# Kernel tuning notes

Hardware: AMD Instinct MI355X
Metric: run time of the kernel (lower is better)

Reference implementation:

```python
import jax, jax.numpy as jnp
import numpy as np

NQ = 10          # qubits
NT = 32          # tokens (LCU terms)
DM = 512         # d_model
DEG = 2          # qsvt degree
B = 128          # batch
NPQC = 4 * NQ    # params per PQC application
DIM = 2 ** NQ    # statevector dimension


def ansatz14_spec(q, layers=1):
    spec = []
    for _ in range(layers):
        spec += [('ry', (i,)) for i in range(q)]
        spec += [('crx', (i, (i + 1) % q)) for i in range(q - 1, -1, -1)]
        spec += [('ry', (i,)) for i in range(q)]
        spec += [('crx', (i, (i - 1) % q)) for i in [q - 1] + list(range(q - 1))]
    return spec

SPEC = ansatz14_spec(NQ, 1)


def _gate_ry(theta):
    h = theta * 0.5
    c = jnp.cos(h)
    s = jnp.sin(h)
    m = jnp.stack([jnp.stack([c, -s], -1), jnp.stack([s, c], -1)], -2)
    return m.astype(jnp.complex64)  # (N,2,2)


def _gate_rx(theta):
    h = theta * 0.5
    c = jnp.cos(h).astype(jnp.complex64)
    s = (-1j) * jnp.sin(h).astype(jnp.complex64)
    return jnp.stack([jnp.stack([c, s], -1), jnp.stack([s, c], -1)], -2)


def _apply_1q(state, mats, wire, q):
    # state: (N, 2^q) complex; mats: (N,2,2); wire 0 is most significant bit
    N = state.shape[0]
    a = 2 ** wire
    bdim = 2 ** (q - wire - 1)
    s = state.reshape(N, a, 2, bdim)
    return jnp.einsum('nij,najb->naib', mats, s).reshape(N, 2 ** q)


def _apply_crx(state, theta, c, t, q):
    # controlled-RX: control wire c, target wire t
    N = state.shape[0]
    st = state.reshape((N,) + (2,) * q)
    ax = 1 + c
    s0 = jnp.take(st, 0, axis=ax)   # control = 0 branch: untouched
    s1 = jnp.take(st, 1, axis=ax)   # control = 1 branch: apply RX on target
    tp = t if t < c else t - 1      # target wire position after removing control axis
    s1n = _apply_1q(s1.reshape(N, -1), _gate_rx(theta), tp, q - 1).reshape(s1.shape)
    return jnp.stack([s0, s1n], axis=ax).reshape(N, 2 ** q)


def _apply_pqc(state, params, q):
    # params: (N, NPQC); fixed small gate list -> Python loop is fine
    for k, (fn, w) in enumerate(SPEC):
        th = params[:, k]
        if fn == 'ry':
            state = _apply_1q(state, _gate_ry(th), w[0], q)
        else:
            state = _apply_crx(state, th, w[0], w[1], q)
    return state


def _apply_lcu(states, params, lcu):
    # states: (B, DIM) complex; params: (B, L, NPQC); lcu: (B, L) complex
    Bn, L = lcu.shape
    rep = jnp.repeat(states, L, axis=0)                    # (B*L, DIM)
    st = _apply_pqc(rep, params.reshape(Bn * L, NPQC), NQ)
    return jnp.einsum('bld,bl->bd', st.reshape(Bn, L, DIM), lcu)


def _measure_xyz(state, q):
    # Pauli expectations per wire: order [X_0..X_{q-1}, Y_0.., Z_0..]
    N = state.shape[0]
    xs, ys, zs = [], [], []
    for w in range(q):
        s = state.reshape(N, 2 ** w, 2, -1)
        a0, a1 = s[:, :, 0, :], s[:, :, 1, :]
        cross = jnp.sum(jnp.conj(a0) * a1, axis=(1, 2))
        xs.append(2.0 * jnp.real(cross))
        ys.append(2.0 * jnp.imag(cross))
        zs.append(jnp.sum(jnp.abs(a0) ** 2 - jnp.abs(a1) ** 2, axis=(1, 2)))
    return jnp.stack(xs + ys + zs, axis=1).astype(jnp.float32)  # (B, 3q)


def reference(tokens_emb, W, b, lcu_re, lcu_im, qsvt_coeffs, ff_params):
    Bn, L, D = tokens_emb.shape
    L = min(L, NT)
    pqc_params = tokens_emb[:, :L] @ W.T + b               # (B, L, NPQC)
    lcu = (lcu_re + 1j * lcu_im).astype(jnp.complex64)[:L]
    lcu = lcu / jnp.sum(jnp.abs(lcu))
    lcu_b = jnp.broadcast_to(lcu[None], (Bn, L))
    init = jnp.zeros((Bn, DIM), jnp.complex64).at[:, 0].set(1.0)
    acc = qsvt_coeffs[0].astype(jnp.complex64) * init
    mono = init
    for k in range(1, DEG + 1):
        mono = _apply_lcu(mono, pqc_params, lcu_b)
        acc = acc + qsvt_coeffs[k].astype(jnp.complex64) * mono
    state = acc / jnp.sum(jnp.abs(qsvt_coeffs))
    state = state / jnp.linalg.norm(state, axis=-1, keepdims=True)
    ffp = jnp.broadcast_to(ff_params[None], (Bn, NPQC))
    state = _apply_pqc(state, ffp, NQ)
    return _measure_xyz(state, NQ)


def setup_inputs():
    key = jax.random.key(0)
    ks = jax.random.split(key, 7)
    return {
        'tokens_emb': jax.random.normal(ks[0], (B, NT, DM), jnp.float32),
        'W': jax.random.normal(ks[1], (NPQC, DM), jnp.float32) * 0.05,
        'b': jax.random.normal(ks[2], (NPQC,), jnp.float32),
        'lcu_re': jax.random.normal(ks[3], (NT,), jnp.float32),
        'lcu_im': jax.random.normal(ks[4], (NT,), jnp.float32),
        'qsvt_coeffs': jax.random.normal(ks[5], (DEG + 1,), jnp.float32),
        'ff_params': jax.random.normal(ks[6], (NPQC,), jnp.float32),
    }
```

## Files before the change

kernel.cpp:

```cpp
#include <hip/hip_runtime.h>
#include <hip/hip_bf16.h>


#define NQ   10
#define NT   32
#define DM   512
#define BATCH 128
#define NPQC 40
#define DIM  1024
#define SLICE_V2F (BATCH * DIM)

typedef float v2f __attribute__((ext_vector_type(2)));

#define WAITLDS asm volatile("s_waitcnt lgkmcnt(0)" ::: "memory")

__device__ __forceinline__ v2f Jrot(v2f v) {
  return __builtin_shufflevector(v, -v, 1, 2);
}
__device__ __forceinline__ v2f Jc(v2f v) {
  return __builtin_shufflevector(-v, v, 1, 2);
}


template<int B>
__device__ __forceinline__ void g_ry(v2f (&a)[16], float c, float s) {
  static_assert(B >= 6, "RY targets must be register bits");
  constexpr int m = 1 << (B - 6);
#pragma unroll
  for (int r = 0; r < 16; ++r) {
    if (!(r & m)) {
      int r1 = r | m;
      v2f a0 = a[r], a1 = a[r1];
      a[r]  = c * a0 - s * a1;
      a[r1] = s * a0 + c * a1;
    }
  }
}

template<int BC, int BT>
__device__ __forceinline__ void g_crx(v2f (&a)[16], int lane, float c, float s) {
  static_assert(BT >= 6, "CRX targets must be register bits");
  constexpr int m = 1 << (BT - 6);
  bool lane_ok = (BC >= 6) || ((lane >> BC) & 1);
  float ce = lane_ok ? c : 1.f;
  float se = lane_ok ? s : 0.f;
#pragma unroll
  for (int r = 0; r < 16; ++r) {
    if (!(r & m)) {
      if constexpr (BC >= 6) { if (!((r >> (BC - 6)) & 1)) continue; }
      int r1 = r | m;
      v2f a0 = a[r], a1 = a[r1];
      a[r]  = ce * a0 + se * Jrot(a1);
      a[r1] = ce * a1 + se * Jrot(a0);
    }
  }
}

template<int L0, int L1, int L2, int L3>
__device__ __forceinline__ void remap(v2f (&a)[16], v2f* __restrict__ slab,
                                      int lane) {
  constexpr int LM = (1 << L0) | (1 << L1) | (1 << L2) | (1 << L3);
#pragma unroll
  for (int r = 0; r < 16; ++r) {
    int f = 0;
    if (L0 < 4 && (r & 1)) f |= 1 << L0;
    if (L1 < 4 && (r & 2)) f |= 1 << L1;
    if (L2 < 4 && (r & 4)) f |= 1 << L2;
    if (L3 < 4 && (r & 8)) f |= 1 << L3;
    slab[r * 64 + (lane ^ f)] = a[r];
  }
  WAITLDS;
  int la = lane & ~LM & 63;
  la |= ((lane >> L0) & 1) << 6;
  la |= ((lane >> L1) & 1) << 7;
  la |= ((lane >> L2) & 1) << 8;
  la |= ((lane >> L3) & 1) << 9;
  if (L0 < 4) la |= ((lane >> L0) & 1) << L0;
  if (L1 < 4) la |= ((lane >> L1) & 1) << L1;
  if (L2 < 4) la |= ((lane >> L2) & 1) << L2;
  if (L3 < 4) la |= ((lane >> L3) & 1) << L3;
#pragma unroll
  for (int r = 0; r < 16; ++r) {
    int rc = ((r & 1) ? (1 << L0) : 0) | ((r & 2) ? (1 << L1) : 0)
           | ((r & 4) ? (1 << L2) : 0) | ((r & 8) ? (1 << L3) : 0);
    a[r] = slab[la ^ rc];
  }
}

template<bool SKIP_HEAD>
__device__ __forceinline__ void apply_pqc_phased(v2f (&a)[16],
    const float2* __restrict__ cs, v2f* __restrict__ slab, int lane) {
#define RYt(B, t)      g_ry<B>(a, t.x, t.y);
#define CXt(BC, BT, t) g_crx<BC, BT>(a, lane, t.x, t.y);
  float2 t10 = cs[10], t11 = cs[11], t12 = cs[12];
  if constexpr (!SKIP_HEAD) {
    float2 t0 = cs[0], t1 = cs[1], t2 = cs[2], t3 = cs[3];
    float2 t4 = cs[4], t5 = cs[5], t6 = cs[6], t7 = cs[7];
    float2 t8 = cs[8], t9 = cs[9];
    RYt(9,t0) RYt(8,t1) RYt(7,t2) RYt(6,t3)
    remap<5,4,3,2>(a, slab, lane);
    RYt(6,t4) RYt(7,t5) RYt(8,t6) RYt(9,t7)
    remap<1,0,2,3>(a, slab, lane);
    RYt(6,t8) RYt(7,t9)
  }
  CXt(7,8,t10) CXt(6,7,t11) CXt(3,6,t12)
  float2 t13 = cs[13], t14 = cs[14], t15 = cs[15], t16 = cs[16];
  remap<1,0,2,3>(a, slab, lane);
  CXt(8,9,t13) CXt(7,8,t14) CXt(6,7,t15) CXt(5,6,t16)
  float2 t17 = cs[17], t18 = cs[18], t19 = cs[19];
  float2 t20 = cs[20], t21 = cs[21], t22 = cs[22], t23 = cs[23];
  remap<2,3,4,5>(a, slab, lane);
  CXt(8,9,t17) CXt(7,8,t18) CXt(6,7,t19)
  RYt(6,t20) RYt(7,t21) RYt(8,t22) RYt(9,t23)
  float2 t24 = cs[24], t25 = cs[25], t26 = cs[26], t27 = cs[27];
  remap<2,3,4,5>(a, slab, lane);
  RYt(6,t24) RYt(7,t25) RYt(8,t26) RYt(9,t27)
  float2 t28 = cs[28], t29 = cs[29];
  float2 t30 = cs[30], t31 = cs[31], t32 = cs[32], t33 = cs[33];
  remap<1,0,2,3>(a, slab, lane);
  RYt(6,t28) RYt(7,t29)
  CXt(7,6,t30) CXt(8,7,t31) CXt(9,8,t32) CXt(4,9,t33)
  float2 t34 = cs[34], t35 = cs[35], t36 = cs[36], t37 = cs[37];
  remap<4,5,1,0>(a, slab, lane);
  CXt(7,6,t34) CXt(8,7,t35) CXt(9,8,t36) CXt(2,9,t37)
  float2 t38 = cs[38], t39 = cs[39];
  remap<2,3,4,5>(a, slab, lane);
  CXt(7,6,t38) CXt(8,7,t39)
#undef RYt
#undef CXt
}

__device__ __forceinline__ int p8_lane_canon(int lane) {
  return (((lane >> 1) & 1) << 9) | ((lane & 1) << 8) | (((lane >> 2) & 1) << 7)
       | (((lane >> 3) & 1) << 6) | (((lane >> 4) & 1) << 5) | (((lane >> 5) & 1) << 4);
}

__device__ __forceinline__ void stagger(int key) {
  int s = key & 3;
  if (s & 1) __builtin_amdgcn_s_sleep(1);
  if (s & 2) __builtin_amdgcn_s_sleep(2);
}

__global__ __launch_bounds__(256) void params_kernel(
    const float* __restrict__ emb, const float* __restrict__ W,
    const float* __restrict__ bias,
    const float* __restrict__ lcu_re, const float* __restrict__ lcu_im,
    const float* __restrict__ ffp,
    float2* __restrict__ cs, float2* __restrict__ ffcs, float2* __restrict__ lcu,
    v2f* __restrict__ part1, v2f* __restrict__ part2) {
  int blk = blockIdx.x;
  int tid = threadIdx.x;
  if (blk >= 257) {
    int idx = (blk - 257) * 256 + tid;
    v2f z = (v2f)(0.f);
    if (idx < SLICE_V2F) part1[idx] = z;
    else                 part2[idx - SLICE_V2F] = z;
    return;
  }
  if (blk == 256) {
    if (tid < NPQC) {
      float h = 0.5f * ffp[tid];
      ffcs[tid] = make_float2(cosf(h), sinf(h));
    }
    if (tid == 64) {
      float ssum = 0.f;
      for (int i = 0; i < NT; ++i) {
        float re = lcu_re[i], im = lcu_im[i];
        ssum += sqrtf(re * re + im * im);
      }
      float inv = 1.f / ssum;
      for (int i = 0; i < NT; ++i)
        lcu[i] = make_float2(lcu_re[i] * inv, lcu_im[i] * inv);
    }
    return;
  }

  __shared__ float Asl[16 * 516];
  int row0 = blk * 16;

  const float4* eg = (const float4*)(emb + (size_t)row0 * DM);
#pragma unroll
  for (int i = 0; i < 8; ++i) {
    int e = tid + i * 256;
    int r = e >> 7, k4 = e & 127;
    float4 v = eg[e];
    *(float4*)&Asl[r * 516 + k4 * 4] = v;
  }
  __syncthreads();

  int kq = tid >> 6;
  int lane = tid & 63;
  int rg = lane >> 3;
  int cg = lane & 7;

  const float* Ar0 = &Asl[(2 * rg) * 516 + kq * 128];
  const float* Ar1 = Ar0 + 516;
  const float* Bg  = W + (size_t)(5 * cg) * DM + kq * 128;

  float acc[2][5] = {};
#pragma unroll 4
  for (int k = 0; k < 128; k += 4) {
    float4 a0 = *(const float4*)(Ar0 + k);
    float4 a1 = *(const float4*)(Ar1 + k);
#pragma unroll
    for (int j = 0; j < 5; ++j) {
      float4 b = *(const float4*)(Bg + j * DM + k);
      acc[0][j] += a0.x * b.x + a0.y * b.y + a0.z * b.z + a0.w * b.w;
      acc[1][j] += a1.x * b.x + a1.y * b.y + a1.z * b.z + a1.w * b.w;
    }
  }

  __syncthreads();
  float* red = Asl;
#pragma unroll
  for (int i = 0; i < 2; ++i)
#pragma unroll
    for (int j = 0; j < 5; ++j)
      red[kq * 644 + (2 * rg + i) * 40 + 5 * cg + j] = acc[i][j];
  __syncthreads();

  for (int o = tid; o < 640; o += 256) {
    float v = bias[o % 40] + red[o] + red[644 + o] + red[1288 + o] + red[1932 + o];
    float h = 0.5f * v;
    cs[(size_t)blk * 640 + o] = make_float2(cosf(h), sinf(h));
  }
}

template<bool FIRST>
__global__ __launch_bounds__(256) void pqc_step(
    const float2* __restrict__ cs, const float2* __restrict__ lcu,
    const v2f* __restrict__ src, v2f* __restrict__ dst) {
  __shared__ v2f slabs[4][1024];
  int tid = threadIdx.x;
  int lane = tid & 63;
  int wvu = __builtin_amdgcn_readfirstlane(tid >> 6);
  int blk = blockIdx.x;
  stagger(blk + wvu);
  int b = blk >> 3, qq = blk & 7;
  int l = qq * 4 + wvu;
  const float2* csrow = cs + (size_t)(b * NT + l) * NPQC;
  v2f* slab = slabs[wvu];

  v2f a[16];
  if constexpr (FIRST) {
    float2 f5 = csrow[5], f4 = csrow[4], f6 = csrow[6], f7 = csrow[7];
    float2 f2 = csrow[2], f3 = csrow[3];
    float2 f8 = csrow[8], f9 = csrow[9], f0 = csrow[0], f1 = csrow[1];
    float lp = ((lane & 1) ? f5.y : f5.x);
    lp *= ((lane & 2) ? f4.y : f4.x);
    lp *= ((lane & 4) ? f6.y : f6.x);
    lp *= ((lane & 8) ? f7.y : f7.x);
    lp *= ((lane & 16) ? f2.y : f2.x);
    lp *= ((lane & 32) ? f3.y : f3.x);
#pragma unroll
    for (int r = 0; r < 16; ++r) {
      float rp = ((r & 1) ? f8.y : f8.x) * ((r & 2) ? f9.y : f9.x)
               * ((r & 4) ? f0.y : f0.x) * ((r & 8) ? f1.y : f1.x);
      a[r].x = lp * rp;
      a[r].y = 0.f;
    }
  } else {
    const v2f* s = src + (size_t)b * DIM;
#pragma unroll
    for (int r = 0; r < 16; ++r) a[r] = s[r * 64 + lane];
  }

  apply_pqc_phased<FIRST>(a, csrow, slab, lane);

  float2 w = lcu[l];
  int pl = p8_lane_canon(lane);
  pl ^= (pl >> 5);
#pragma unroll
  for (int r = 0; r < 16; ++r) {
    int rc = ((r & 1) << 3) | ((r & 2) << 1) | ((r & 4) >> 1) | ((r & 8) >> 3);
    slab[pl ^ rc] = w.x * a[r] + w.y * Jc(a[r]);
  }
  __syncthreads();

  float* df = (float*)(dst + (size_t)b * DIM);
#pragma unroll
  for (int i = 0; i < 4; ++i) {
    int n = tid + i * 256;
    int ph = n ^ (n >> 5);
    v2f sum = slabs[0][ph] + slabs[1][ph] + slabs[2][ph] + slabs[3][ph];
    atomicAdd(df + 2 * n,     sum.x);
    atomicAdd(df + 2 * n + 1, sum.y);
  }
}

__global__ __launch_bounds__(256) void final_fused(
    const v2f* __restrict__ red1, const v2f* __restrict__ red2b,
    const float* __restrict__ qsvt, const float2* __restrict__ ffcs,
    float* __restrict__ out) {
  __shared__ v2f st[1024];
  __shared__ float2 ang[40];
  __shared__ float rbuf[4];
  __shared__ float red2[120];
  int b = blockIdx.x, tid = threadIdx.x;
  int lane = tid & 63, wvu = tid >> 6;
  float q0 = qsvt[0], q1 = qsvt[1], q2 = qsvt[2];
  const v2f* r1 = red1 + (size_t)b * DIM;
  const v2f* p2 = red2b + (size_t)b * DIM;

  if (tid < NPQC) ang[tid] = ffcs[tid];

  v2f vals[4];
  float nn = 0.f;
#pragma unroll
  for (int i = 0; i < 4; ++i) {
    int n = tid + i * 256;
    v2f v = q1 * r1[n] + q2 * p2[n];
    if (n == 0) v.x += q0;
    vals[i] = v;
    nn += v.x * v.x + v.y * v.y;
  }
#pragma unroll
  for (int o = 1; o < 64; o <<= 1) nn += __shfl_xor(nn, o);
  if (lane == 0) rbuf[wvu] = nn;
  __syncthreads();
  float inv = 1.f / sqrtf(rbuf[0] + rbuf[1] + rbuf[2] + rbuf[3]);
#pragma unroll
  for (int i = 0; i < 4; ++i) {
    int n = tid + i * 256;
    st[n ^ (n >> 5)] = vals[i] * inv;
  }
  __syncthreads();

#pragma unroll 1
  for (int k = 0; k < NPQC; ++k) {
    int isCrx, c, t;
    if (k < 10)      { isCrx = 0; t = k;      c = 0; }
    else if (k < 20) { int i = 19 - k; isCrx = 1; c = i; t = (i == 9) ? 0 : i + 1; }
    else if (k < 30) { isCrx = 0; t = k - 20; c = 0; }
    else             { int i = (k == 30) ? 9 : k - 31; isCrx = 1; c = i; t = (i == 0) ? 9 : i - 1; }
    int m  = 1 << (9 - t);
    int cb = 9 - c;
    float2 th = ang[k];
    float cg = th.x, sg = th.y;

    v2f a0[2], a1[2];
    int j0[2], j1[2], en[2];
#pragma unroll
    for (int p = 0; p < 2; ++p) {
      int qp = p * 256 + tid;
      int i0 = ((qp & ~(m - 1)) << 1) | (qp & (m - 1));
      int i1 = i0 | m;
      j0[p] = i0 ^ (i0 >> 5);
      j1[p] = i1 ^ (i1 >> 5);
      en[p] = (i0 >> cb) & 1;
      a0[p] = st[j0[p]];
      a1[p] = st[j1[p]];
    }
#pragma unroll
    for (int p = 0; p < 2; ++p) {
      v2f n0, n1;
      if (!isCrx) {
        n0 = cg * a0[p] - sg * a1[p];
        n1 = sg * a0[p] + cg * a1[p];
      } else {
        float ce = en[p] ? cg : 1.f;
        float se = en[p] ? sg : 0.f;
        n0 = ce * a0[p] + se * Jrot(a1[p]);
        n1 = ce * a1[p] + se * Jrot(a0[p]);
      }
      st[j0[p]] = n0;
      st[j1[p]] = n1;
    }
    __syncthreads();
  }

  float prt[30];
#pragma unroll
  for (int w = 0; w < NQ; ++w) {
    int m = 1 << (9 - w);
    float xr = 0.f, xi = 0.f, zz = 0.f;
#pragma unroll
    for (int p = 0; p < 2; ++p) {
      int qp = p * 256 + tid;
      int i0 = ((qp & ~(m - 1)) << 1) | (qp & (m - 1));
      int i1 = i0 | m;
      v2f a0 = st[i0 ^ (i0 >> 5)];
      v2f a1 = st[i1 ^ (i1 >> 5)];
      xr += a0.x * a1.x + a0.y * a1.y;
      xi += a0.x * a1.y - a0.y * a1.x;
      zz += a0.x * a0.x + a0.y * a0.y - a1.x * a1.x - a1.y * a1.y;
    }
    prt[w]      = xr;
    prt[10 + w] = xi;
    prt[20 + w] = zz;
  }
#pragma unroll
  for (int v = 0; v < 30; ++v) {
#pragma unroll
    for (int o = 1; o < 64; o <<= 1) prt[v] += __shfl_xor(prt[v], o);
  }
  if (lane == 0) {
#pragma unroll
    for (int v = 0; v < 30; ++v) red2[wvu * 30 + v] = prt[v];
  }
  __syncthreads();
  if (tid < 30) {
    float s2 = red2[tid] + red2[30 + tid] + red2[60 + tid] + red2[90 + tid];
    float sc = (tid < 20) ? 2.f : 1.f;
    out[b * 30 + tid] = sc * s2;
  }
}


extern "C" void kernel_launch(void* const* d_in, const int* in_sizes, int n_in,
                              void* d_out, int out_size, void* d_ws, size_t ws_size,
                              hipStream_t stream) {
  const float* emb    = (const float*)d_in[0];
  const float* W      = (const float*)d_in[1];
  const float* bias   = (const float*)d_in[2];
  const float* lcu_re = (const float*)d_in[3];
  const float* lcu_im = (const float*)d_in[4];
  const float* qsvt   = (const float*)d_in[5];
  const float* ffp    = (const float*)d_in[6];
  float* out = (float*)d_out;

  char* ws = (char*)d_ws;
  float2* cs    = (float2*)ws;
  float2* ffcs  = (float2*)(ws + 1310720);
  float2* lcu   = (float2*)(ws + 1311040);
  v2f*    part1 = (v2f*)(ws + 1311744);
  v2f*    part2 = (v2f*)(ws + 1311744 + 1048576);

  params_kernel<<<1281, 256, 0, stream>>>(emb, W, bias, lcu_re, lcu_im, ffp,
                                          cs, ffcs, lcu, part1, part2);
  pqc_step<true><<<1024, 256, 0, stream>>>(cs, lcu, nullptr, part1);
  pqc_step<false><<<1024, 256, 0, stream>>>(cs, lcu, part1, part2);
  final_fused<<<BATCH, 256, 0, stream>>>(part1, part2, qsvt, ffcs, out);
}
```

Before: 148.3 us.

## Replace LDS remap-phased circuit with runtime gate loop using cross-lane shuffles

Replaces the statically scheduled PQC application, which periodically remapped qubit bits between lanes and registers through LDS, with a non-unrolled runtime loop over the 40 gates. Gates on register bits use templated register kernels chosen by switch, and gates on lane bits use __shfl_xor exchanges. This removes the LDS remap traffic and the stagger sleeps, but adds a runtime gate-decode loop with branches, and many shuffles (16 registers × 2 floats per lane-bit gate) that may cost more than the removed remaps. The canonical layout is now fixed, so the initial product state and the final LDS store order are adjusted to match.

```diff
diff --git a/kernel.cpp b/kernel.cpp
--- a/kernel.cpp
+++ b/kernel.cpp
@@ -12,8 +12,6 @@
 
 typedef float v2f __attribute__((ext_vector_type(2)));
 
-#define WAITLDS asm volatile("s_waitcnt lgkmcnt(0)" ::: "memory")
-
 __device__ __forceinline__ v2f Jrot(v2f v) {
   return __builtin_shufflevector(v, -v, 1, 2);
 }
@@ -22,14 +20,12 @@
 }
 
 
-template<int B>
-__device__ __forceinline__ void g_ry(v2f (&a)[16], float c, float s) {
-  static_assert(B >= 6, "RY targets must be register bits");
-  constexpr int m = 1 << (B - 6);
+template<int M>
+__device__ __forceinline__ void ry_reg(v2f (&a)[16], float c, float s) {
 #pragma unroll
   for (int r = 0; r < 16; ++r) {
-    if (!(r & m)) {
-      int r1 = r | m;
+    if (!(r & M)) {
+      int r1 = r | M;
       v2f a0 = a[r], a1 = a[r1];
       a[r]  = c * a0 - s * a1;
       a[r1] = s * a0 + c * a1;
@@ -37,18 +33,16 @@
   }
 }
 
-template<int BC, int BT>
-__device__ __forceinline__ void g_crx(v2f (&a)[16], int lane, float c, float s) {
-  static_assert(BT >= 6, "CRX targets must be register bits");
-  constexpr int m = 1 << (BT - 6);
-  bool lane_ok = (BC >= 6) || ((lane >> BC) & 1);
-  float ce = lane_ok ? c : 1.f;
-  float se = lane_ok ? s : 0.f;
+template<int M>
+__device__ __forceinline__ void crx_reg(v2f (&a)[16], int lane, int cb,
+                                        float c, float s) {
 #pragma unroll
   for (int r = 0; r < 16; ++r) {
-    if (!(r & m)) {
-      if constexpr (BC >= 6) { if (!((r >> (BC - 6)) & 1)) continue; }
-      int r1 = r | m;
+    if (!(r & M)) {
+      int r1 = r | M;
+      int en = (cb >= 6) ? ((r >> (cb - 6)) & 1) : ((lane >> cb) & 1);
+      float ce = en ? c : 1.f;
+      float se = en ? s : 0.f;
       v2f a0 = a[r], a1 = a[r1];
       a[r]  = ce * a0 + se * Jrot(a1);
       a[r1] = ce * a1 + se * Jrot(a0);
@@ -56,89 +50,80 @@
   }
 }
 
-template<int L0, int L1, int L2, int L3>
-__device__ __forceinline__ void remap(v2f (&a)[16], v2f* __restrict__ slab,
-                                      int lane) {
-  constexpr int LM = (1 << L0) | (1 << L1) | (1 << L2) | (1 << L3);
-#pragma unroll
-  for (int r = 0; r < 16; ++r) {
-    int f = 0;
-    if (L0 < 4 && (r & 1)) f |= 1 << L0;
-    if (L1 < 4 && (r & 2)) f |= 1 << L1;
-    if (L2 < 4 && (r & 4)) f |= 1 << L2;
-    if (L3 < 4 && (r & 8)) f |= 1 << L3;
-    slab[r * 64 + (lane ^ f)] = a[r];
-  }
-  WAITLDS;
-  int la = lane & ~LM & 63;
-  la |= ((lane >> L0) & 1) << 6;
-  la |= ((lane >> L1) & 1) << 7;
-  la |= ((lane >> L2) & 1) << 8;
-  la |= ((lane >> L3) & 1) << 9;
-  if (L0 < 4) la |= ((lane >> L0) & 1) << L0;
-  if (L1 < 4) la |= ((lane >> L1) & 1) << L1;
-  if (L2 < 4) la |= ((lane >> L2) & 1) << L2;
-  if (L3 < 4) la |= ((lane >> L3) & 1) << L3;
-#pragma unroll
-  for (int r = 0; r < 16; ++r) {
-    int rc = ((r & 1) ? (1 << L0) : 0) | ((r & 2) ? (1 << L1) : 0)
-           | ((r & 4) ? (1 << L2) : 0) | ((r & 8) ? (1 << L3) : 0);
-    a[r] = slab[la ^ rc];
-  }
-}
-
-template<bool SKIP_HEAD>
-__device__ __forceinline__ void apply_pqc_phased(v2f (&a)[16],
-    const float2* __restrict__ cs, v2f* __restrict__ slab, int lane) {
-#define RYt(B, t)      g_ry<B>(a, t.x, t.y);
-#define CXt(BC, BT, t) g_crx<BC, BT>(a, lane, t.x, t.y);
-  float2 t10 = cs[10], t11 = cs[11], t12 = cs[12];
-  if constexpr (!SKIP_HEAD) {
-    float2 t0 = cs[0], t1 = cs[1], t2 = cs[2], t3 = cs[3];
-    float2 t4 = cs[4], t5 = cs[5], t6 = cs[6], t7 = cs[7];
-    float2 t8 = cs[8], t9 = cs[9];
-    RYt(9,t0) RYt(8,t1) RYt(7,t2) RYt(6,t3)
-    remap<5,4,3,2>(a, slab, lane);
-    RYt(6,t4) RYt(7,t5) RYt(8,t6) RYt(9,t7)
-    remap<1,0,2,3>(a, slab, lane);
-    RYt(6,t8) RYt(7,t9)
-  }
-  CXt(7,8,t10) CXt(6,7,t11) CXt(3,6,t12)
-  float2 t13 = cs[13], t14 = cs[14], t15 = cs[15], t16 = cs[16];
-  remap<1,0,2,3>(a, slab, lane);
-  CXt(8,9,t13) CXt(7,8,t14) CXt(6,7,t15) CXt(5,6,t16)
-  float2 t17 = cs[17], t18 = cs[18], t19 = cs[19];
-  float2 t20 = cs[20], t21 = cs[21], t22 = cs[22], t23 = cs[23];
-  remap<2,3,4,5>(a, slab, lane);
-  CXt(8,9,t17) CXt(7,8,t18) CXt(6,7,t19)
-  RYt(6,t20) RYt(7,t21) RYt(8,t22) RYt(9,t23)
-  float2 t24 = cs[24], t25 = cs[25], t26 = cs[26], t27 = cs[27];
-  remap<2,3,4,5>(a, slab, lane);
-  RYt(6,t24) RYt(7,t25) RYt(8,t26) RYt(9,t27)
-  float2 t28 = cs[28], t29 = cs[29];
-  float2 t30 = cs[30], t31 = cs[31], t32 = cs[32], t33 = cs[33];
-  remap<1,0,2,3>(a, slab, lane);
-  RYt(6,t28) RYt(7,t29)
-  CXt(7,6,t30) CXt(8,7,t31) CXt(9,8,t32) CXt(4,9,t33)
-  float2 t34 = cs[34], t35 = cs[35], t36 = cs[36], t37 = cs[37];
-  remap<4,5,1,0>(a, slab, lane);
-  CXt(7,6,t34) CXt(8,7,t35) CXt(9,8,t36) CXt(2,9,t37)
-  float2 t38 = cs[38], t39 = cs[39];
-  remap<2,3,4,5>(a, slab, lane);
-  CXt(7,6,t38) CXt(8,7,t39)
-#undef RYt
-#undef CXt
-}
-
-__device__ __forceinline__ int p8_lane_canon(int lane) {
-  return (((lane >> 1) & 1) << 9) | ((lane & 1) << 8) | (((lane >> 2) & 1) << 7)
-       | (((lane >> 3) & 1) << 6) | (((lane >> 4) & 1) << 5) | (((lane >> 5) & 1) << 4);
-}
-
-__device__ __forceinline__ void stagger(int key) {
-  int s = key & 3;
-  if (s & 1) __builtin_amdgcn_s_sleep(1);
-  if (s & 2) __builtin_amdgcn_s_sleep(2);
+template<int K0>
+__device__ __forceinline__ void run_circuit(v2f (&a)[16],
+    const float2* __restrict__ angs, int lane) {
+  float2 th = angs[K0];
+#pragma unroll 1
+  for (int k = K0; k < NPQC; ++k) {
+    float2 thn = angs[(k + 1 < NPQC) ? k + 1 : k];
+    int isCrx, tb, cb;
+    {
+      int c, t;
+      if (k < 10)      { isCrx = 0; t = k;      c = 0; }
+      else if (k < 20) { int i = 19 - k; isCrx = 1; c = i; t = (i == 9) ? 0 : i + 1; }
+      else if (k < 30) { isCrx = 0; t = k - 20; c = 0; }
+      else             { int i = (k == 30) ? 9 : k - 31; isCrx = 1; c = i; t = (i == 0) ? 9 : i - 1; }
+      tb = 9 - t;
+      cb = 9 - c;
+    }
+    float cg = th.x, sg = th.y;
+
+    if (tb >= 6) {
+      if (!isCrx) {
+        switch (tb) {
+          case 6:  ry_reg<1>(a, cg, sg); break;
+          case 7:  ry_reg<2>(a, cg, sg); break;
+          case 8:  ry_reg<4>(a, cg, sg); break;
+          default: ry_reg<8>(a, cg, sg); break;
+        }
+      } else {
+        switch (tb) {
+          case 6:  crx_reg<1>(a, lane, cb, cg, sg); break;
+          case 7:  crx_reg<2>(a, lane, cb, cg, sg); break;
+          case 8:  crx_reg<4>(a, lane, cb, cg, sg); break;
+          default: crx_reg<8>(a, lane, cb, cg, sg); break;
+        }
+      }
+    } else {
+      int lm = 1 << tb;
+      if (!isCrx) {
+        int bit = (lane >> tb) & 1;
+        float ss = bit ? sg : -sg;
+#pragma unroll
+        for (int r = 0; r < 16; ++r) {
+          float px = __shfl_xor(a[r].x, lm);
+          float py = __shfl_xor(a[r].y, lm);
+          a[r].x = cg * a[r].x + ss * px;
+          a[r].y = cg * a[r].y + ss * py;
+        }
+      } else if (cb < 6) {
+        int en = (lane >> cb) & 1;
+        float ce = en ? cg : 1.f;
+        float se = en ? sg : 0.f;
+#pragma unroll
+        for (int r = 0; r < 16; ++r) {
+          float px = __shfl_xor(a[r].x, lm);
+          float py = __shfl_xor(a[r].y, lm);
+          a[r].x = ce * a[r].x + se * py;
+          a[r].y = ce * a[r].y - se * px;
+        }
+      } else {
+        int csh = cb - 6;
+#pragma unroll
+        for (int r = 0; r < 16; ++r) {
+          float px = __shfl_xor(a[r].x, lm);
+          float py = __shfl_xor(a[r].y, lm);
+          int en = (r >> csh) & 1;
+          float ce = en ? cg : 1.f;
+          float se = en ? sg : 0.f;
+          a[r].x = ce * a[r].x + se * py;
+          a[r].y = ce * a[r].y - se * px;
+        }
+      }
+    }
+    th = thn;
+  }
 }
 
 __global__ __launch_bounds__(256) void params_kernel(
@@ -235,7 +220,6 @@
   int lane = tid & 63;
   int wvu = __builtin_amdgcn_readfirstlane(tid >> 6);
   int blk = blockIdx.x;
-  stagger(blk + wvu);
   int b = blk >> 3, qq = blk & 7;
   int l = qq * 4 + wvu;
   const float2* csrow = cs + (size_t)(b * NT + l) * NPQC;
@@ -243,19 +227,19 @@
 
   v2f a[16];
   if constexpr (FIRST) {
-    float2 f5 = csrow[5], f4 = csrow[4], f6 = csrow[6], f7 = csrow[7];
-    float2 f2 = csrow[2], f3 = csrow[3];
-    float2 f8 = csrow[8], f9 = csrow[9], f0 = csrow[0], f1 = csrow[1];
-    float lp = ((lane & 1) ? f5.y : f5.x);
-    lp *= ((lane & 2) ? f4.y : f4.x);
-    lp *= ((lane & 4) ? f6.y : f6.x);
-    lp *= ((lane & 8) ? f7.y : f7.x);
-    lp *= ((lane & 16) ? f2.y : f2.x);
-    lp *= ((lane & 32) ? f3.y : f3.x);
+    float2 f9 = csrow[9], f8 = csrow[8], f7 = csrow[7], f6 = csrow[6];
+    float2 f5 = csrow[5], f4 = csrow[4], f3 = csrow[3], f2 = csrow[2];
+    float2 f1 = csrow[1], f0 = csrow[0];
+    float lp = ((lane & 1) ? f9.y : f9.x);
+    lp *= ((lane & 2)  ? f8.y : f8.x);
+    lp *= ((lane & 4)  ? f7.y : f7.x);
+    lp *= ((lane & 8)  ? f6.y : f6.x);
+    lp *= ((lane & 16) ? f5.y : f5.x);
+    lp *= ((lane & 32) ? f4.y : f4.x);
 #pragma unroll
     for (int r = 0; r < 16; ++r) {
-      float rp = ((r & 1) ? f8.y : f8.x) * ((r & 2) ? f9.y : f9.x)
-               * ((r & 4) ? f0.y : f0.x) * ((r & 8) ? f1.y : f1.x);
+      float rp = ((r & 1) ? f3.y : f3.x) * ((r & 2) ? f2.y : f2.x)
+               * ((r & 4) ? f1.y : f1.x) * ((r & 8) ? f0.y : f0.x);
       a[r].x = lp * rp;
       a[r].y = 0.f;
     }
@@ -265,15 +249,13 @@
     for (int r = 0; r < 16; ++r) a[r] = s[r * 64 + lane];
   }
 
-  apply_pqc_phased<FIRST>(a, csrow, slab, lane);
+  run_circuit<FIRST ? 10 : 0>(a, csrow, lane);
 
   float2 w = lcu[l];
-  int pl = p8_lane_canon(lane);
-  pl ^= (pl >> 5);
 #pragma unroll
   for (int r = 0; r < 16; ++r) {
-    int rc = ((r & 1) << 3) | ((r & 2) << 1) | ((r & 4) >> 1) | ((r & 8) >> 3);
-    slab[pl ^ rc] = w.x * a[r] + w.y * Jc(a[r]);
+    int n = r * 64 + lane;
+    slab[n ^ (n >> 5)] = w.x * a[r] + w.y * Jc(a[r]);
   }
   __syncthreads();
 
```

After: 193.0 us. 1.3x slower.

## Fuse final PQC and measurement into second pqc_step via last-block counter

Applied to the files above, without the earlier changes.

Removes the separate final kernel by having the last of the eight blocks per batch row, detected with an atomic counter, run the normalization, feed-forward PQC and measurement inside the second pqc_step. The counters are zeroed in params_kernel. This saves a kernel launch and the gap between kernels, and lets the tail work for one batch row overlap with other rows still accumulating. In exchange it adds a threadfence, atomic reads of the accumulated buffer, and a serialized tail inside the last block of each row.

```diff
diff --git a/kernel.cpp b/kernel.cpp
--- a/kernel.cpp
+++ b/kernel.cpp
@@ -147,7 +147,7 @@
     const float* __restrict__ lcu_re, const float* __restrict__ lcu_im,
     const float* __restrict__ ffp,
     float2* __restrict__ cs, float2* __restrict__ ffcs, float2* __restrict__ lcu,
-    v2f* __restrict__ part1, v2f* __restrict__ part2) {
+    v2f* __restrict__ part1, v2f* __restrict__ part2, int* __restrict__ cnt) {
   int blk = blockIdx.x;
   int tid = threadIdx.x;
   if (blk >= 257) {
@@ -162,6 +162,7 @@
       float h = 0.5f * ffp[tid];
       ffcs[tid] = make_float2(cosf(h), sinf(h));
     }
+    if (tid >= 128) cnt[tid - 128] = 0;
     if (tid == 64) {
       float ssum = 0.f;
       for (int i = 0; i < NT; ++i) {
@@ -229,8 +230,11 @@
 template<bool FIRST>
 __global__ __launch_bounds__(256) void pqc_step(
     const float2* __restrict__ cs, const float2* __restrict__ lcu,
-    const v2f* __restrict__ src, v2f* __restrict__ dst) {
+    const v2f* __restrict__ src, v2f* __restrict__ dst,
+    const float* __restrict__ qsvt, const float2* __restrict__ ffcs,
+    float* __restrict__ out, int* __restrict__ cnt) {
   __shared__ v2f slabs[4][1024];
+  __shared__ int lastFlag;
   int tid = threadIdx.x;
   int lane = tid & 63;
   int wvu = __builtin_amdgcn_readfirstlane(tid >> 6);
@@ -286,123 +290,131 @@
     atomicAdd(df + 2 * n,     sum.x);
     atomicAdd(df + 2 * n + 1, sum.y);
   }
-}
-
-__global__ __launch_bounds__(256) void final_fused(
-    const v2f* __restrict__ red1, const v2f* __restrict__ red2b,
-    const float* __restrict__ qsvt, const float2* __restrict__ ffcs,
-    float* __restrict__ out) {
-  __shared__ v2f st[1024];
-  __shared__ float2 ang[40];
-  __shared__ float rbuf[4];
-  __shared__ float red2[120];
-  int b = blockIdx.x, tid = threadIdx.x;
-  int lane = tid & 63, wvu = tid >> 6;
-  float q0 = qsvt[0], q1 = qsvt[1], q2 = qsvt[2];
-  const v2f* r1 = red1 + (size_t)b * DIM;
-  const v2f* p2 = red2b + (size_t)b * DIM;
-
-  if (tid < NPQC) ang[tid] = ffcs[tid];
-
-  v2f vals[4];
-  float nn = 0.f;
-#pragma unroll
-  for (int i = 0; i < 4; ++i) {
-    int n = tid + i * 256;
-    v2f v = q1 * r1[n] + q2 * p2[n];
-    if (n == 0) v.x += q0;
-    vals[i] = v;
-    nn += v.x * v.x + v.y * v.y;
-  }
-#pragma unroll
-  for (int o = 1; o < 64; o <<= 1) nn += __shfl_xor(nn, o);
-  if (lane == 0) rbuf[wvu] = nn;
-  __syncthreads();
-  float inv = 1.f / sqrtf(rbuf[0] + rbuf[1] + rbuf[2] + rbuf[3]);
-#pragma unroll
-  for (int i = 0; i < 4; ++i) {
-    int n = tid + i * 256;
-    st[n ^ (n >> 5)] = vals[i] * inv;
-  }
-  __syncthreads();
+
+  if constexpr (!FIRST) {
+    __threadfence();
+    if (tid == 0) {
+      int old = atomicAdd(&cnt[b], 1);
+      lastFlag = (old == 7);
+    }
+    __syncthreads();
+    if (!lastFlag) return;
+
+    v2f* st = slabs[0];
+    float* aux = (float*)slabs[1];
+    float2* ang = (float2*)aux;
+    float* rbuf = aux + 80;
+    float* red2 = aux + 96;
+
+    if (tid < NPQC) ang[tid] = ffcs[tid];
+    float q0 = qsvt[0], q1 = qsvt[1], q2 = qsvt[2];
+    const v2f* r1 = src + (size_t)b * DIM;
+
+    v2f vals[4];
+    float nn = 0.f;
+#pragma unroll
+    for (int i = 0; i < 4; ++i) {
+      int n = tid + i * 256;
+      float mx = atomicAdd(df + 2 * n,     0.f);
+      float my = atomicAdd(df + 2 * n + 1, 0.f);
+      v2f r = r1[n];
+      v2f v;
+      v.x = q1 * r.x + q2 * mx;
+      v.y = q1 * r.y + q2 * my;
+      if (n == 0) v.x += q0;
+      vals[i] = v;
+      nn += v.x * v.x + v.y * v.y;
+    }
+#pragma unroll
+    for (int o = 1; o < 64; o <<= 1) nn += __shfl_xor(nn, o);
+    if (lane == 0) rbuf[wvu] = nn;
+    __syncthreads();
+    float inv = 1.f / sqrtf(rbuf[0] + rbuf[1] + rbuf[2] + rbuf[3]);
+#pragma unroll
+    for (int i = 0; i < 4; ++i) {
+      int n = tid + i * 256;
+      st[n ^ (n >> 5)] = vals[i] * inv;
+    }
+    __syncthreads();
 
 #pragma unroll 1
-  for (int k = 0; k < NPQC; ++k) {
-    int isCrx, c, t;
-    if (k < 10)      { isCrx = 0; t = k;      c = 0; }
-    else if (k < 20) { int i = 19 - k; isCrx = 1; c = i; t = (i == 9) ? 0 : i + 1; }
-    else if (k < 30) { isCrx = 0; t = k - 20; c = 0; }
-    else             { int i = (k == 30) ? 9 : k - 31; isCrx = 1; c = i; t = (i == 0) ? 9 : i - 1; }
-    int m  = 1 << (9 - t);
-    int cb = 9 - c;
-    float2 th = ang[k];
-    float cg = th.x, sg = th.y;
-
-    v2f a0[2], a1[2];
-    int j0[2], j1[2], en[2];
-#pragma unroll
-    for (int p = 0; p < 2; ++p) {
-      int qp = p * 256 + tid;
-      int i0 = ((qp & ~(m - 1)) << 1) | (qp & (m - 1));
-      int i1 = i0 | m;
-      j0[p] = i0 ^ (i0 >> 5);
-      j1[p] = i1 ^ (i1 >> 5);
-      en[p] = (i0 >> cb) & 1;
-      a0[p] = st[j0[p]];
-      a1[p] = st[j1[p]];
-    }
-#pragma unroll
-    for (int p = 0; p < 2; ++p) {
-      v2f n0, n1;
-      if (!isCrx) {
-        n0 = cg * a0[p] - sg * a1[p];
-        n1 = sg * a0[p] + cg * a1[p];
-      } else {
-        float ce = en[p] ? cg : 1.f;
-        float se = en[p] ? sg : 0.f;
-        n0 = ce * a0[p] + se * Jrot(a1[p]);
-        n1 = ce * a1[p] + se * Jrot(a0[p]);
+    for (int k = 0; k < NPQC; ++k) {
+      int isCrx, c, t;
+      if (k < 10)      { isCrx = 0; t = k;      c = 0; }
+      else if (k < 20) { int i = 19 - k; isCrx = 1; c = i; t = (i == 9) ? 0 : i + 1; }
+      else if (k < 30) { isCrx = 0; t = k - 20; c = 0; }
+      else             { int i = (k == 30) ? 9 : k - 31; isCrx = 1; c = i; t = (i == 0) ? 9 : i - 1; }
+      int m  = 1 << (9 - t);
+      int cb = 9 - c;
+      float2 th = ang[k];
+      float cg = th.x, sg = th.y;
+
+      v2f a0[2], a1[2];
+      int j0[2], j1[2], en[2];
+#pragma unroll
+      for (int p = 0; p < 2; ++p) {
+        int qp = p * 256 + tid;
+        int i0 = ((qp & ~(m - 1)) << 1) | (qp & (m - 1));
+        int i1 = i0 | m;
+        j0[p] = i0 ^ (i0 >> 5);
+        j1[p] = i1 ^ (i1 >> 5);
+        en[p] = (i0 >> cb) & 1;
+        a0[p] = st[j0[p]];
+        a1[p] = st[j1[p]];
       }
-      st[j0[p]] = n0;
-      st[j1[p]] = n1;
+#pragma unroll
+      for (int p = 0; p < 2; ++p) {
+        v2f n0, n1;
+        if (!isCrx) {
+          n0 = cg * a0[p] - sg * a1[p];
+          n1 = sg * a0[p] + cg * a1[p];
+        } else {
+          float ce = en[p] ? cg : 1.f;
+          float se = en[p] ? sg : 0.f;
+          n0 = ce * a0[p] + se * Jrot(a1[p]);
+          n1 = ce * a1[p] + se * Jrot(a0[p]);
+        }
+        st[j0[p]] = n0;
+        st[j1[p]] = n1;
+      }
+      __syncthreads();
+    }
+
+    float prt[30];
+#pragma unroll
+    for (int w2 = 0; w2 < NQ; ++w2) {
+      int m = 1 << (9 - w2);
+      float xr = 0.f, xi = 0.f, zz = 0.f;
+#pragma unroll
+      for (int p = 0; p < 2; ++p) {
+        int qp = p * 256 + tid;
+        int i0 = ((qp & ~(m - 1)) << 1) | (qp & (m - 1));
+        int i1 = i0 | m;
+        v2f a0 = st[i0 ^ (i0 >> 5)];
+        v2f a1 = st[i1 ^ (i1 >> 5)];
+        xr += a0.x * a1.x + a0.y * a1.y;
+        xi += a0.x * a1.y - a0.y * a1.x;
+        zz += a0.x * a0.x + a0.y * a0.y - a1.x * a1.x - a1.y * a1.y;
+      }
+      prt[w2]      = xr;
+      prt[10 + w2] = xi;
+      prt[20 + w2] = zz;
+    }
+#pragma unroll
+    for (int v = 0; v < 30; ++v) {
+#pragma unroll
+      for (int o = 1; o < 64; o <<= 1) prt[v] += __shfl_xor(prt[v], o);
+    }
+    if (lane == 0) {
+#pragma unroll
+      for (int v = 0; v < 30; ++v) red2[wvu * 30 + v] = prt[v];
     }
     __syncthreads();
-  }
-
-  float prt[30];
-#pragma unroll
-  for (int w = 0; w < NQ; ++w) {
-    int m = 1 << (9 - w);
-    float xr = 0.f, xi = 0.f, zz = 0.f;
-#pragma unroll
-    for (int p = 0; p < 2; ++p) {
-      int qp = p * 256 + tid;
-      int i0 = ((qp & ~(m - 1)) << 1) | (qp & (m - 1));
-      int i1 = i0 | m;
-      v2f a0 = st[i0 ^ (i0 >> 5)];
-      v2f a1 = st[i1 ^ (i1 >> 5)];
-      xr += a0.x * a1.x + a0.y * a1.y;
-      xi += a0.x * a1.y - a0.y * a1.x;
-      zz += a0.x * a0.x + a0.y * a0.y - a1.x * a1.x - a1.y * a1.y;
-    }
-    prt[w]      = xr;
-    prt[10 + w] = xi;
-    prt[20 + w] = zz;
-  }
-#pragma unroll
-  for (int v = 0; v < 30; ++v) {
-#pragma unroll
-    for (int o = 1; o < 64; o <<= 1) prt[v] += __shfl_xor(prt[v], o);
-  }
-  if (lane == 0) {
-#pragma unroll
-    for (int v = 0; v < 30; ++v) red2[wvu * 30 + v] = prt[v];
-  }
-  __syncthreads();
-  if (tid < 30) {
-    float s2 = red2[tid] + red2[30 + tid] + red2[60 + tid] + red2[90 + tid];
-    float sc = (tid < 20) ? 2.f : 1.f;
-    out[b * 30 + tid] = sc * s2;
+    if (tid < 30) {
+      float s2 = red2[tid] + red2[30 + tid] + red2[60 + tid] + red2[90 + tid];
+      float sc = (tid < 20) ? 2.f : 1.f;
+      out[b * 30 + tid] = sc * s2;
+    }
   }
 }
 
@@ -425,10 +437,12 @@
   float2* lcu   = (float2*)(ws + 1311040);
   v2f*    part1 = (v2f*)(ws + 1311744);
   v2f*    part2 = (v2f*)(ws + 1311744 + 1048576);
+  int*    cnt   = (int*)(ws + 1311744 + 2 * 1048576);
 
   params_kernel<<<1281, 256, 0, stream>>>(emb, W, bias, lcu_re, lcu_im, ffp,
-                                          cs, ffcs, lcu, part1, part2);
-  pqc_step<true><<<1024, 256, 0, stream>>>(cs, lcu, nullptr, part1);
-  pqc_step<false><<<1024, 256, 0, stream>>>(cs, lcu, part1, part2);
-  final_fused<<<BATCH, 256, 0, stream>>>(part1, part2, qsvt, ffcs, out);
-}
+                                          cs, ffcs, lcu, part1, part2, cnt);
+  pqc_step<true><<<1024, 256, 0, stream>>>(cs, lcu, nullptr, part1,
+                                           qsvt, ffcs, out, cnt);
+  pqc_step<false><<<1024, 256, 0, stream>>>(cs, lcu, part1, part2,
+                                            qsvt, ffcs, out, cnt);
+}
```

New measurement: 204.8 us. 38.0% more time.
